# Kernel tuning notes

Measured on AMD Instinct MI355X. Metric: run time of the kernel, lower is better.

Reference implementation:

```python
import jax, jax.numpy as jnp
import numpy as np

B, T, D_IN = 64, 512, 512
D_HID, D_OUT = 1024, 512
NUM_DAYS = 24
EPS = 1e-5


def setup_inputs() -> dict:
    key = jax.random.key(0)
    ks = jax.random.split(key, 8)
    x = jax.random.normal(ks[0], (B, T, D_IN), dtype=jnp.float32)
    day_indices = jax.random.randint(ks[1], (B,), 0, NUM_DAYS)
    s1 = 1.0 / np.sqrt(D_IN)
    s2 = 1.0 / np.sqrt(D_HID)
    W1 = jax.random.uniform(ks[2], (NUM_DAYS, D_IN, D_HID), jnp.float32, -s1, s1)
    b1 = jax.random.uniform(ks[3], (NUM_DAYS, D_HID), jnp.float32, -s1, s1)
    W2 = jax.random.uniform(ks[4], (NUM_DAYS, D_HID, D_OUT), jnp.float32, -s2, s2)
    b2 = jax.random.uniform(ks[5], (NUM_DAYS, D_OUT), jnp.float32, -s2, s2)
    gamma = jnp.ones((NUM_DAYS, D_OUT), jnp.float32)
    beta = jnp.zeros((NUM_DAYS, D_OUT), jnp.float32)
    return {"x": x, "day_indices": day_indices, "W1": W1, "b1": b1,
            "W2": W2, "b2": b2, "gamma": gamma, "beta": beta}


def reference(x, day_indices, W1, b1, W2, b2, gamma, beta):
    # Gather each sample's day-specific adapter params, then one batched pass.
    # Equivalent to the per-day mask/gather/scatter loop in the torch module.
    # Dropout is identity (eval mode).
    W1d = W1[day_indices]                      # [B, D_in, D_hid]
    b1d = b1[day_indices][:, None, :]          # [B, 1, D_hid]
    W2d = W2[day_indices]                      # [B, D_hid, D_out]
    b2d = b2[day_indices][:, None, :]          # [B, 1, D_out]
    h = jax.nn.relu(jnp.einsum('btd,bdh->bth', x, W1d) + b1d)
    y = jnp.einsum('bth,bho->bto', h, W2d) + b2d
    # per-day LayerNorm over last dim
    mean = jnp.mean(y, axis=-1, keepdims=True)
    var = jnp.var(y, axis=-1, keepdims=True)
    y_hat = (y - mean) * jax.lax.rsqrt(var + EPS)
    g = gamma[day_indices][:, None, :]
    bt = beta[day_indices][:, None, :]
    return y_hat * g + bt
```

## Files before the change

kernel.cpp:

```cpp
#include <hip/hip_runtime.h>

#define B_    64
#define T_    512
#define DIN   512
#define DHID  1024
#define DOUT  512
#define NDAYS 24

typedef unsigned short u16;
typedef __bf16 bf16x8 __attribute__((ext_vector_type(8)));
typedef u16    u16x8  __attribute__((ext_vector_type(8)));
typedef float  f32x4  __attribute__((ext_vector_type(4)));

static __device__ __forceinline__ u16 f2bf(float f) {
    union { float f; unsigned u; } v; v.f = f;
    unsigned r = v.u + 0x7FFFu + ((v.u >> 16) & 1u);
    return (u16)(r >> 16);
}
static __device__ __forceinline__ float bf2f(u16 h) {
    union { unsigned u; float f; } v; v.u = ((unsigned)h) << 16;
    return v.f;
}

static __device__ __forceinline__ void gload_lds16(const void* g, void* l) {
    __builtin_amdgcn_global_load_lds(
        (const __attribute__((address_space(1))) void*)g,
        (__attribute__((address_space(3))) void*)l, 16, 0, 0);
}

__global__ __launch_bounds__(256)
void transpose_w(const float* __restrict__ W, u16* __restrict__ WT, int R, int C) {
    __shared__ float t[32][33];
    const int d  = blockIdx.z;
    const int r0 = blockIdx.y * 32, c0 = blockIdx.x * 32;
    const int tx = threadIdx.x, ty = threadIdx.y;
    const float* Wd = W + (size_t)d * R * C;
    u16* WTd = WT + (size_t)d * R * C;
#pragma unroll
    for (int i = 0; i < 4; ++i)
        t[ty + i * 8][tx] = Wd[(size_t)(r0 + ty + i * 8) * C + c0 + tx];
    __syncthreads();
#pragma unroll
    for (int i = 0; i < 4; ++i)
        WTd[(size_t)(c0 + ty + i * 8) * R + r0 + tx] = f2bf(t[tx][ty + i * 8]);
}

__global__ __launch_bounds__(256)
void cvt_bf16(const float* __restrict__ in, u16* __restrict__ outp, int n8) {
    int i = blockIdx.x * 256 + threadIdx.x;
    const int stride = gridDim.x * 256;
    for (; i < n8; i += stride) {
        float4 a = ((const float4*)in)[i * 2];
        float4 b = ((const float4*)in)[i * 2 + 1];
        u16x8 p;
        p[0] = f2bf(a.x); p[1] = f2bf(a.y); p[2] = f2bf(a.z); p[3] = f2bf(a.w);
        p[4] = f2bf(b.x); p[5] = f2bf(b.y); p[6] = f2bf(b.z); p[7] = f2bf(b.w);
        ((u16x8*)outp)[i] = p;
    }
}

template<int MT, int NT, int KT, bool RELU, bool OUT_BF16>
__global__ __launch_bounds__(512, 1)
void gemm8(const u16* __restrict__ Aall,
           const u16* __restrict__ BT,
           const float* __restrict__ bias,
           const int* __restrict__ didx,
           void* __restrict__ Call)
{
    constexpr int GX = MT / 256;
    constexpr int GY = NT / 256;
    constexpr int NWG = GX * GY * B_;
    constexpr int NT_K = KT / 64;
    static_assert(NT_K >= 2 && (NWG % 8) == 0, "geometry");

    constexpr int Q = NWG / 8;
    const int hw = blockIdx.x;
    const int l  = (hw & 7) * Q + (hw >> 3);
    const int bx = l % GX;
    const int by = (l / GX) % GY;
    const int bz = l / (GX * GY);

    const int day = didx[bz];
    const int m0 = bx * 256, n0 = by * 256;
    const int tid = threadIdx.x;
    const int wv = tid >> 6, ln = tid & 63;
    const int wm = wv >> 2, wn = wv & 3;

    __shared__ __align__(16) u16 sA[2][256 * 64];
    __shared__ __align__(16) u16 sB[2][256 * 64];

    const u16* Ab = Aall + (size_t)bz * MT * KT + (size_t)m0 * KT;
    const u16* Bt = BT + (size_t)day * NT * KT + (size_t)n0 * KT;

    auto stageA = [&](int buf, int t, int h) {
#pragma unroll
        for (int c = 0; c < 2; ++c) {
            const int rl = h * 128 + wv * 16 + c * 8 + (ln >> 3);
            const int cd = (ln & 7) ^ (rl & 7);
            gload_lds16(Ab + (size_t)rl * KT + t * 64 + cd * 8,
                        (char*)&sA[buf][(h * 128 + wv * 16 + c * 8) * 64]);
        }
    };
    auto stageB = [&](int buf, int t, int h) {
#pragma unroll
        for (int c = 0; c < 2; ++c) {
            const int rl = h * 128 + wv * 16 + c * 8 + (ln >> 3);
            const int cd = (ln & 7) ^ (rl & 7);
            gload_lds16(Bt + (size_t)rl * KT + t * 64 + cd * 8,
                        (char*)&sB[buf][(h * 128 + wv * 16 + c * 8) * 64]);
        }
    };

    f32x4 acc[8][4];
#pragma unroll
    for (int i = 0; i < 8; ++i)
#pragma unroll
        for (int j = 0; j < 4; ++j)
            acc[i][j] = (f32x4){0.f, 0.f, 0.f, 0.f};

    stageA(0, 0, 0); stageB(0, 0, 0); stageA(0, 0, 1); stageB(0, 0, 1);
    stageA(1, 1, 0); stageB(1, 1, 0);
    asm volatile("s_waitcnt vmcnt(4)" ::: "memory");
    __builtin_amdgcn_s_barrier();

    for (int t = 0; t < NT_K; ++t) {
        const int buf = t & 1;
        const u16* sAb = sA[buf];
        const u16* sBb = sB[buf];
        bf16x8 av[2][4], bv[2][2];

#pragma unroll
        for (int p = 0; p < 4; ++p) {
            const int mq = p >> 1, nq = p & 1;
            if (p == 0 || p == 2) {
#pragma unroll
                for (int ks = 0; ks < 2; ++ks)
#pragma unroll
                    for (int mi = 0; mi < 4; ++mi) {
                        const int r = mq * 128 + wm * 64 + mi * 16 + (ln & 15);
                        const int slot = (ks * 4 + (ln >> 4)) ^ (r & 7);
                        av[ks][mi] = *(const bf16x8*)&sAb[r * 64 + slot * 8];
                    }
            }
#pragma unroll
            for (int ks = 0; ks < 2; ++ks)
#pragma unroll
                for (int ni = 0; ni < 2; ++ni) {
                    const int r = nq * 128 + wn * 32 + ni * 16 + (ln & 15);
                    const int slot = (ks * 4 + (ln >> 4)) ^ (r & 7);
                    bv[ks][ni] = *(const bf16x8*)&sBb[r * 64 + slot * 8];
                }
            if (p == 0)      { if (t + 1 < NT_K) stageA(buf ^ 1, t + 1, 1); }
            else if (p == 1) { if (t + 1 < NT_K) stageB(buf ^ 1, t + 1, 1); }
            else if (p == 2) { if (t + 2 < NT_K) stageA(buf, t + 2, 0); }
            else             { if (t + 2 < NT_K) stageB(buf, t + 2, 0); }

            __builtin_amdgcn_s_barrier();
            asm volatile("s_waitcnt lgkmcnt(0)" ::: "memory");
            __builtin_amdgcn_sched_barrier(0);
            __builtin_amdgcn_s_setprio(1);
#pragma unroll
            for (int ks = 0; ks < 2; ++ks)
#pragma unroll
                for (int mi = 0; mi < 4; ++mi)
#pragma unroll
                    for (int ni = 0; ni < 2; ++ni)
                        acc[mq * 4 + mi][nq * 2 + ni] =
                            __builtin_amdgcn_mfma_f32_16x16x32_bf16(
                                av[ks][mi], bv[ks][ni],
                                acc[mq * 4 + mi][nq * 2 + ni], 0, 0, 0);
            __builtin_amdgcn_s_setprio(0);
            if (p == 3) {
                if (t + 2 < NT_K) asm volatile("s_waitcnt vmcnt(4)" ::: "memory");
                else              asm volatile("s_waitcnt vmcnt(0)" ::: "memory");
            }
            __builtin_amdgcn_s_barrier();
        }
    }

    const float* bs = bias + (size_t)day * NT + n0;
#pragma unroll
    for (int nq = 0; nq < 2; ++nq)
#pragma unroll
        for (int ni = 0; ni < 2; ++ni) {
            const int col = nq * 128 + wn * 32 + ni * 16 + (ln & 15);
            const float bval = bs[col];
#pragma unroll
            for (int mq = 0; mq < 2; ++mq)
#pragma unroll
                for (int mi = 0; mi < 4; ++mi)
#pragma unroll
                    for (int i = 0; i < 4; ++i) {
                        const int row = mq * 128 + wm * 64 + mi * 16 + (ln >> 4) * 4 + i;
                        float v = acc[mq * 4 + mi][nq * 2 + ni][i] + bval;
                        if (RELU) v = fmaxf(v, 0.f);
                        const size_t off = (size_t)bz * MT * NT + (size_t)(m0 + row) * NT + (n0 + col);
                        if (OUT_BF16) ((u16*)Call)[off] = f2bf(v);
                        else          ((float*)Call)[off] = v;
                    }
        }
}

__global__ __launch_bounds__(512, 1)
void gemm2_ln(const u16* __restrict__ Aall,
              const u16* __restrict__ BT,
              const float* __restrict__ bias,
              const int* __restrict__ didx,
              const float* __restrict__ gamma,
              const float* __restrict__ beta,
              float* __restrict__ out)
{
    constexpr int BM = 128, BK = 64;
    constexpr int KT = DHID;
    constexpr int NT_K = KT / BK;
    constexpr int GX = T_ / BM;
    constexpr int NWG = GX * B_;

    constexpr int Q = NWG / 8;
    const int hw = blockIdx.x;
    const int l  = (hw & 7) * Q + (hw >> 3);
    const int bx = l % GX;
    const int bz = l / GX;

    const int day = didx[bz];
    const int m0 = bx * BM;
    const int tid = threadIdx.x;
    const int wv = tid >> 6, ln = tid & 63;
    const int wm = wv >> 2, wn = wv & 3;

    __shared__ __align__(16) u16 sA[2][BM * BK];
    __shared__ __align__(16) u16 sB[2][DOUT * BK];

    const u16* Ab = Aall + (size_t)bz * T_ * KT + (size_t)m0 * KT;
    const u16* Bt = BT + (size_t)day * DOUT * KT;

    auto stageA = [&](int buf, int t) {
#pragma unroll
        for (int c = 0; c < 2; ++c) {
            const int rl = wv * 16 + c * 8 + (ln >> 3);
            const int cd = (ln & 7) ^ (rl & 7);
            gload_lds16(Ab + (size_t)rl * KT + t * BK + cd * 8,
                        (char*)&sA[buf][(wv * 16 + c * 8) * BK]);
        }
    };
    auto stageBh = [&](int buf, int t, int h) {
#pragma unroll
        for (int c = 0; c < 4; ++c) {
            const int rl = h * 256 + wv * 32 + c * 8 + (ln >> 3);
            const int cd = (ln & 7) ^ (rl & 7);
            gload_lds16(Bt + (size_t)rl * KT + t * BK + cd * 8,
                        (char*)&sB[buf][(h * 256 + wv * 32 + c * 8) * BK]);
        }
    };

    f32x4 acc[4][8];
#pragma unroll
    for (int i = 0; i < 4; ++i)
#pragma unroll
        for (int j = 0; j < 8; ++j)
            acc[i][j] = (f32x4){0.f, 0.f, 0.f, 0.f};

    stageA(0, 0); stageBh(0, 0, 0); stageBh(0, 0, 1);
    stageA(1, 1); stageBh(1, 1, 0);
    asm volatile("s_waitcnt vmcnt(6)" ::: "memory");
    __builtin_amdgcn_s_barrier();

    for (int t = 0; t < NT_K; ++t) {
        const int buf = t & 1;
        const u16* sAb = sA[buf];
        const u16* sBb = sB[buf];
        bf16x8 av[2][4], bv[2][2];

#pragma unroll
        for (int p = 0; p < 4; ++p) {
            if (p == 0) {
#pragma unroll
                for (int ks = 0; ks < 2; ++ks)
#pragma unroll
                    for (int mi = 0; mi < 4; ++mi) {
                        const int r = wm * 64 + mi * 16 + (ln & 15);
                        const int slot = (ks * 4 + (ln >> 4)) ^ (r & 7);
                        av[ks][mi] = *(const bf16x8*)&sAb[r * BK + slot * 8];
                    }
            }
#pragma unroll
            for (int ks = 0; ks < 2; ++ks)
#pragma unroll
                for (int ni = 0; ni < 2; ++ni) {
                    const int r = p * 128 + wn * 32 + ni * 16 + (ln & 15);
                    const int slot = (ks * 4 + (ln >> 4)) ^ (r & 7);
                    bv[ks][ni] = *(const bf16x8*)&sBb[r * BK + slot * 8];
                }
            if (p == 0)      { if (t + 1 < NT_K) stageBh(buf ^ 1, t + 1, 1); }
            else if (p == 1) { if (t + 2 < NT_K) stageA(buf, t + 2); }
            else if (p == 2) { if (t + 2 < NT_K) stageBh(buf, t + 2, 0); }

            __builtin_amdgcn_s_barrier();
            asm volatile("s_waitcnt lgkmcnt(0)" ::: "memory");
            __builtin_amdgcn_sched_barrier(0);
            __builtin_amdgcn_s_setprio(1);
#pragma unroll
            for (int ks = 0; ks < 2; ++ks)
#pragma unroll
                for (int mi = 0; mi < 4; ++mi)
#pragma unroll
                    for (int ni = 0; ni < 2; ++ni)
                        acc[mi][p * 2 + ni] =
                            __builtin_amdgcn_mfma_f32_16x16x32_bf16(
                                av[ks][mi], bv[ks][ni], acc[mi][p * 2 + ni], 0, 0, 0);
            __builtin_amdgcn_s_setprio(0);
            if (p == 3) {
                if (t + 2 < NT_K) asm volatile("s_waitcnt vmcnt(6)" ::: "memory");
                else              asm volatile("s_waitcnt vmcnt(0)" ::: "memory");
            }
            __builtin_amdgcn_s_barrier();
        }
    }

    const float* bs = bias + (size_t)day * DOUT;
    float bval[8];
#pragma unroll
    for (int f = 0; f < 8; ++f)
        bval[f] = bs[(f >> 1) * 128 + wn * 32 + (f & 1) * 16 + (ln & 15)];

    u16* yb = (u16*)&sB[0][0];
#pragma unroll
    for (int mi = 0; mi < 4; ++mi)
#pragma unroll
        for (int f = 0; f < 8; ++f) {
            const int col = (f >> 1) * 128 + wn * 32 + (f & 1) * 16 + (ln & 15);
#pragma unroll
            for (int i = 0; i < 4; ++i) {
                const int rloc = wm * 64 + mi * 16 + (ln >> 4) * 4 + i;
                yb[rloc * DOUT + col] = f2bf(acc[mi][f][i] + bval[f]);
            }
        }
    __syncthreads();

    const float* gs = gamma + (size_t)day * DOUT;
    const float* es = beta + (size_t)day * DOUT;
    const float4 g0 = ((const float4*)gs)[ln * 2];
    const float4 g1 = ((const float4*)gs)[ln * 2 + 1];
    const float4 e0 = ((const float4*)es)[ln * 2];
    const float4 e1 = ((const float4*)es)[ln * 2 + 1];

    float* op = out + (size_t)bz * T_ * DOUT + (size_t)m0 * DOUT;
#pragma unroll 4
    for (int r = wv * 16; r < wv * 16 + 16; ++r) {
        const u16x8 yv = *(const u16x8*)&yb[r * DOUT + ln * 8];
        float yf[8];
#pragma unroll
        for (int j = 0; j < 8; ++j) yf[j] = bf2f(yv[j]);
        float s = 0.f, q = 0.f;
#pragma unroll
        for (int j = 0; j < 8; ++j) { s += yf[j]; q += yf[j] * yf[j]; }
#pragma unroll
        for (int o = 32; o; o >>= 1) { s += __shfl_xor(s, o); q += __shfl_xor(q, o); }
        const float mean = s * (1.f / 512.f);
        const float var  = q * (1.f / 512.f) - mean * mean;
        const float rstd = rsqrtf(var + 1e-5f);
        float4 o0, o1;
        o0.x = (yf[0] - mean) * rstd * g0.x + e0.x;
        o0.y = (yf[1] - mean) * rstd * g0.y + e0.y;
        o0.z = (yf[2] - mean) * rstd * g0.z + e0.z;
        o0.w = (yf[3] - mean) * rstd * g0.w + e0.w;
        o1.x = (yf[4] - mean) * rstd * g1.x + e1.x;
        o1.y = (yf[5] - mean) * rstd * g1.y + e1.y;
        o1.z = (yf[6] - mean) * rstd * g1.z + e1.z;
        o1.w = (yf[7] - mean) * rstd * g1.w + e1.w;
        ((float4*)(op + (size_t)r * DOUT))[ln * 2] = o0;
        ((float4*)(op + (size_t)r * DOUT))[ln * 2 + 1] = o1;
    }
}

extern "C" void kernel_launch(void* const* d_in, const int* in_sizes, int n_in,
                              void* d_out, int out_size, void* d_ws, size_t ws_size,
                              hipStream_t stream)
{
    const float* x     = (const float*)d_in[0];
    const int*   didx  = (const int*)d_in[1];
    const float* W1    = (const float*)d_in[2];
    const float* b1    = (const float*)d_in[3];
    const float* W2    = (const float*)d_in[4];
    const float* b2    = (const float*)d_in[5];
    const float* gamma = (const float*)d_in[6];
    const float* beta  = (const float*)d_in[7];
    float* out = (float*)d_out;

    char* ws = (char*)d_ws;
    u16* W1T = (u16*)ws;
    u16* h   = (u16*)(ws + 25165824);
    u16* xb  = (u16*)(ws + 92274688);
    u16* W2T = xb;

    transpose_w<<<dim3(DHID / 32, DIN / 32, NDAYS), dim3(32, 8), 0, stream>>>(W1, W1T, DIN, DHID);
    cvt_bf16<<<2048, 256, 0, stream>>>(x, xb, B_ * T_ * DIN / 8);

    gemm8<T_, DHID, DIN, true, true>
        <<<dim3(2 * 4 * B_), 512, 0, stream>>>(xb, W1T, b1, didx, h);

    transpose_w<<<dim3(DOUT / 32, DHID / 32, NDAYS), dim3(32, 8), 0, stream>>>(W2, W2T, DHID, DOUT);

    gemm2_ln<<<dim3(4 * B_), 512, 0, stream>>>(h, W2T, b2, didx, gamma, beta, out);
}
```

Measured before the change: 155.8 us.

## Fuse fp32-to-bf16 conversion of x into first GEMM's A-tile load path

```diff
diff --git a/kernel.cpp b/kernel.cpp
--- a/kernel.cpp
+++ b/kernel.cpp
@@ -45,33 +45,18 @@
         WTd[(size_t)(c0 + ty + i * 8) * R + r0 + tx] = f2bf(t[tx][ty + i * 8]);
 }
 
-__global__ __launch_bounds__(256)
-void cvt_bf16(const float* __restrict__ in, u16* __restrict__ outp, int n8) {
-    int i = blockIdx.x * 256 + threadIdx.x;
-    const int stride = gridDim.x * 256;
-    for (; i < n8; i += stride) {
-        float4 a = ((const float4*)in)[i * 2];
-        float4 b = ((const float4*)in)[i * 2 + 1];
-        u16x8 p;
-        p[0] = f2bf(a.x); p[1] = f2bf(a.y); p[2] = f2bf(a.z); p[3] = f2bf(a.w);
-        p[4] = f2bf(b.x); p[5] = f2bf(b.y); p[6] = f2bf(b.z); p[7] = f2bf(b.w);
-        ((u16x8*)outp)[i] = p;
-    }
-}
-
-template<int MT, int NT, int KT, bool RELU, bool OUT_BF16>
 __global__ __launch_bounds__(512, 1)
-void gemm8(const u16* __restrict__ Aall,
-           const u16* __restrict__ BT,
-           const float* __restrict__ bias,
-           const int* __restrict__ didx,
-           void* __restrict__ Call)
+void gemm1_x(const float* __restrict__ X,
+             const u16* __restrict__ BT,
+             const float* __restrict__ bias,
+             const int* __restrict__ didx,
+             u16* __restrict__ H)
 {
+    constexpr int MT = T_, NT = DHID, KT = DIN;
     constexpr int GX = MT / 256;
     constexpr int GY = NT / 256;
     constexpr int NWG = GX * GY * B_;
     constexpr int NT_K = KT / 64;
-    static_assert(NT_K >= 2 && (NWG % 8) == 0, "geometry");
 
     constexpr int Q = NWG / 8;
     const int hw = blockIdx.x;
@@ -89,16 +74,35 @@
     __shared__ __align__(16) u16 sA[2][256 * 64];
     __shared__ __align__(16) u16 sB[2][256 * 64];
 
-    const u16* Ab = Aall + (size_t)bz * MT * KT + (size_t)m0 * KT;
+    const float* Af = X + (size_t)bz * MT * KT + (size_t)m0 * KT;
     const u16* Bt = BT + (size_t)day * NT * KT + (size_t)n0 * KT;
 
-    auto stageA = [&](int buf, int t, int h) {
-#pragma unroll
-        for (int c = 0; c < 2; ++c) {
-            const int rl = h * 128 + wv * 16 + c * 8 + (ln >> 3);
-            const int cd = (ln & 7) ^ (rl & 7);
-            gload_lds16(Ab + (size_t)rl * KT + t * 64 + cd * 8,
-                        (char*)&sA[buf][(h * 128 + wv * 16 + c * 8) * 64]);
+    int aR[4], aS[4];
+    const float* aSrc[4];
+#pragma unroll
+    for (int i = 0; i < 4; ++i) {
+        const int chunk = i * 512 + tid;
+        const int r = chunk >> 3, s = chunk & 7, cd = s ^ (r & 7);
+        aR[i] = r; aS[i] = s;
+        aSrc[i] = Af + (size_t)r * KT + cd * 8;
+    }
+    auto loadA = [&](f32x4 a[4][2], int t) {
+#pragma unroll
+        for (int i = 0; i < 4; ++i) {
+            a[i][0] = *(const f32x4*)(aSrc[i] + t * 64);
+            a[i][1] = *(const f32x4*)(aSrc[i] + t * 64 + 4);
+        }
+    };
+    auto writeA = [&](f32x4 a[4][2], int buf) {
+#pragma unroll
+        for (int i = 0; i < 4; ++i) {
+            u16x8 v;
+#pragma unroll
+            for (int j = 0; j < 4; ++j) {
+                v[j]     = f2bf(a[i][0][j]);
+                v[4 + j] = f2bf(a[i][1][j]);
+            }
+            *(u16x8*)&sA[buf][aR[i] * 64 + aS[i] * 8] = v;
         }
     };
     auto stageB = [&](int buf, int t, int h) {
@@ -118,11 +122,18 @@
         for (int j = 0; j < 4; ++j)
             acc[i][j] = (f32x4){0.f, 0.f, 0.f, 0.f};
 
-    stageA(0, 0, 0); stageB(0, 0, 0); stageA(0, 0, 1); stageB(0, 0, 1);
-    stageA(1, 1, 0); stageB(1, 1, 0);
-    asm volatile("s_waitcnt vmcnt(4)" ::: "memory");
+    f32x4 aP[4][2], aQ[4][2];
+    loadA(aP, 0);
+    stageB(0, 0, 0); stageB(0, 0, 1);
+    loadA(aQ, 1);
+    stageB(1, 1, 0);
+    asm volatile("s_waitcnt vmcnt(0)" ::: "memory");
+    writeA(aP, 0);
+    writeA(aQ, 1);
+    asm volatile("s_waitcnt lgkmcnt(0)" ::: "memory");
     __builtin_amdgcn_s_barrier();
 
+    f32x4 aN[4][2];
     for (int t = 0; t < NT_K; ++t) {
         const int buf = t & 1;
         const u16* sAb = sA[buf];
@@ -150,10 +161,9 @@
                     const int slot = (ks * 4 + (ln >> 4)) ^ (r & 7);
                     bv[ks][ni] = *(const bf16x8*)&sBb[r * 64 + slot * 8];
                 }
-            if (p == 0)      { if (t + 1 < NT_K) stageA(buf ^ 1, t + 1, 1); }
-            else if (p == 1) { if (t + 1 < NT_K) stageB(buf ^ 1, t + 1, 1); }
-            else if (p == 2) { if (t + 2 < NT_K) stageA(buf, t + 2, 0); }
-            else             { if (t + 2 < NT_K) stageB(buf, t + 2, 0); }
+            if (p == 0)      { if (t + 1 < NT_K) stageB(buf ^ 1, t + 1, 1); }
+            else if (p == 1) { if (t + 2 < NT_K) loadA(aN, t + 2); }
+            else if (p == 3) { if (t + 2 < NT_K) stageB(buf, t + 2, 0); }
 
             __builtin_amdgcn_s_barrier();
             asm volatile("s_waitcnt lgkmcnt(0)" ::: "memory");
@@ -171,8 +181,12 @@
                                 acc[mq * 4 + mi][nq * 2 + ni], 0, 0, 0);
             __builtin_amdgcn_s_setprio(0);
             if (p == 3) {
-                if (t + 2 < NT_K) asm volatile("s_waitcnt vmcnt(4)" ::: "memory");
-                else              asm volatile("s_waitcnt vmcnt(0)" ::: "memory");
+                if (t + 2 < NT_K) {
+                    asm volatile("s_waitcnt vmcnt(2)" ::: "memory");
+                    writeA(aN, buf);
+                } else {
+                    asm volatile("s_waitcnt vmcnt(0)" ::: "memory");
+                }
             }
             __builtin_amdgcn_s_barrier();
         }
@@ -192,11 +206,8 @@
 #pragma unroll
                     for (int i = 0; i < 4; ++i) {
                         const int row = mq * 128 + wm * 64 + mi * 16 + (ln >> 4) * 4 + i;
-                        float v = acc[mq * 4 + mi][nq * 2 + ni][i] + bval;
-                        if (RELU) v = fmaxf(v, 0.f);
-                        const size_t off = (size_t)bz * MT * NT + (size_t)(m0 + row) * NT + (n0 + col);
-                        if (OUT_BF16) ((u16*)Call)[off] = f2bf(v);
-                        else          ((float*)Call)[off] = v;
+                        const float v = fmaxf(acc[mq * 4 + mi][nq * 2 + ni][i] + bval, 0.f);
+                        H[(size_t)bz * MT * NT + (size_t)(m0 + row) * NT + (n0 + col)] = f2bf(v);
                     }
         }
 }
@@ -390,16 +401,12 @@
     char* ws = (char*)d_ws;
     u16* W1T = (u16*)ws;
     u16* h   = (u16*)(ws + 25165824);
-    u16* xb  = (u16*)(ws + 92274688);
-    u16* W2T = xb;
+    u16* W2T = (u16*)(ws + 92274688);
 
     transpose_w<<<dim3(DHID / 32, DIN / 32, NDAYS), dim3(32, 8), 0, stream>>>(W1, W1T, DIN, DHID);
-    cvt_bf16<<<2048, 256, 0, stream>>>(x, xb, B_ * T_ * DIN / 8);
-
-    gemm8<T_, DHID, DIN, true, true>
-        <<<dim3(2 * 4 * B_), 512, 0, stream>>>(xb, W1T, b1, didx, h);
-
     transpose_w<<<dim3(DOUT / 32, DHID / 32, NDAYS), dim3(32, 8), 0, stream>>>(W2, W2T, DHID, DOUT);
 
+    gemm1_x<<<dim3(2 * 4 * B_), 512, 0, stream>>>(x, W1T, b1, didx, h);
+
     gemm2_ln<<<dim3(4 * B_), 512, 0, stream>>>(h, W2T, b2, didx, gamma, beta, out);
 }
```

Result: slower. 162.9 us (+4.6%).

## Halve GEMM1 K-tile to 32 so two workgroups fit per CU

Applied to the files above, without the earlier changes.

```diff
diff --git a/kernel.cpp b/kernel.cpp
--- a/kernel.cpp
+++ b/kernel.cpp
@@ -60,17 +60,17 @@
 }
 
 template<int MT, int NT, int KT, bool RELU, bool OUT_BF16>
-__global__ __launch_bounds__(512, 1)
-void gemm8(const u16* __restrict__ Aall,
-           const u16* __restrict__ BT,
-           const float* __restrict__ bias,
-           const int* __restrict__ didx,
-           void* __restrict__ Call)
+__global__ __launch_bounds__(512, 2)
+void gemm8k32(const u16* __restrict__ Aall,
+              const u16* __restrict__ BT,
+              const float* __restrict__ bias,
+              const int* __restrict__ didx,
+              void* __restrict__ Call)
 {
     constexpr int GX = MT / 256;
     constexpr int GY = NT / 256;
     constexpr int NWG = GX * GY * B_;
-    constexpr int NT_K = KT / 64;
+    constexpr int NT_K = KT / 32;
     static_assert(NT_K >= 2 && (NWG % 8) == 0, "geometry");
 
     constexpr int Q = NWG / 8;
@@ -86,29 +86,23 @@
     const int wv = tid >> 6, ln = tid & 63;
     const int wm = wv >> 2, wn = wv & 3;
 
-    __shared__ __align__(16) u16 sA[2][256 * 64];
-    __shared__ __align__(16) u16 sB[2][256 * 64];
+    __shared__ __align__(16) u16 sA[2][256 * 32];
+    __shared__ __align__(16) u16 sB[2][256 * 32];
 
     const u16* Ab = Aall + (size_t)bz * MT * KT + (size_t)m0 * KT;
     const u16* Bt = BT + (size_t)day * NT * KT + (size_t)n0 * KT;
 
     auto stageA = [&](int buf, int t, int h) {
-#pragma unroll
-        for (int c = 0; c < 2; ++c) {
-            const int rl = h * 128 + wv * 16 + c * 8 + (ln >> 3);
-            const int cd = (ln & 7) ^ (rl & 7);
-            gload_lds16(Ab + (size_t)rl * KT + t * 64 + cd * 8,
-                        (char*)&sA[buf][(h * 128 + wv * 16 + c * 8) * 64]);
-        }
+        const int rl = h * 128 + wv * 16 + (ln >> 2);
+        const int cd = (ln & 3) ^ (rl & 3);
+        gload_lds16(Ab + (size_t)rl * KT + t * 32 + cd * 8,
+                    (char*)&sA[buf][(h * 128 + wv * 16) * 32]);
     };
     auto stageB = [&](int buf, int t, int h) {
-#pragma unroll
-        for (int c = 0; c < 2; ++c) {
-            const int rl = h * 128 + wv * 16 + c * 8 + (ln >> 3);
-            const int cd = (ln & 7) ^ (rl & 7);
-            gload_lds16(Bt + (size_t)rl * KT + t * 64 + cd * 8,
-                        (char*)&sB[buf][(h * 128 + wv * 16 + c * 8) * 64]);
-        }
+        const int rl = h * 128 + wv * 16 + (ln >> 2);
+        const int cd = (ln & 3) ^ (rl & 3);
+        gload_lds16(Bt + (size_t)rl * KT + t * 32 + cd * 8,
+                    (char*)&sB[buf][(h * 128 + wv * 16) * 32]);
     };
 
     f32x4 acc[8][4];
@@ -120,36 +114,32 @@
 
     stageA(0, 0, 0); stageB(0, 0, 0); stageA(0, 0, 1); stageB(0, 0, 1);
     stageA(1, 1, 0); stageB(1, 1, 0);
-    asm volatile("s_waitcnt vmcnt(4)" ::: "memory");
+    asm volatile("s_waitcnt vmcnt(2)" ::: "memory");
     __builtin_amdgcn_s_barrier();
 
     for (int t = 0; t < NT_K; ++t) {
         const int buf = t & 1;
         const u16* sAb = sA[buf];
         const u16* sBb = sB[buf];
-        bf16x8 av[2][4], bv[2][2];
+        bf16x8 av[4], bv[2];
 
 #pragma unroll
         for (int p = 0; p < 4; ++p) {
             const int mq = p >> 1, nq = p & 1;
             if (p == 0 || p == 2) {
 #pragma unroll
-                for (int ks = 0; ks < 2; ++ks)
-#pragma unroll
-                    for (int mi = 0; mi < 4; ++mi) {
-                        const int r = mq * 128 + wm * 64 + mi * 16 + (ln & 15);
-                        const int slot = (ks * 4 + (ln >> 4)) ^ (r & 7);
-                        av[ks][mi] = *(const bf16x8*)&sAb[r * 64 + slot * 8];
-                    }
-            }
-#pragma unroll
-            for (int ks = 0; ks < 2; ++ks)
-#pragma unroll
-                for (int ni = 0; ni < 2; ++ni) {
-                    const int r = nq * 128 + wn * 32 + ni * 16 + (ln & 15);
-                    const int slot = (ks * 4 + (ln >> 4)) ^ (r & 7);
-                    bv[ks][ni] = *(const bf16x8*)&sBb[r * 64 + slot * 8];
+                for (int mi = 0; mi < 4; ++mi) {
+                    const int r = mq * 128 + wm * 64 + mi * 16 + (ln & 15);
+                    const int slot = (ln >> 4) ^ (r & 3);
+                    av[mi] = *(const bf16x8*)&sAb[r * 32 + slot * 8];
                 }
+            }
+#pragma unroll
+            for (int ni = 0; ni < 2; ++ni) {
+                const int r = nq * 128 + wn * 32 + ni * 16 + (ln & 15);
+                const int slot = (ln >> 4) ^ (r & 3);
+                bv[ni] = *(const bf16x8*)&sBb[r * 32 + slot * 8];
+            }
             if (p == 0)      { if (t + 1 < NT_K) stageA(buf ^ 1, t + 1, 1); }
             else if (p == 1) { if (t + 1 < NT_K) stageB(buf ^ 1, t + 1, 1); }
             else if (p == 2) { if (t + 2 < NT_K) stageA(buf, t + 2, 0); }
@@ -160,18 +150,16 @@
             __builtin_amdgcn_sched_barrier(0);
             __builtin_amdgcn_s_setprio(1);
 #pragma unroll
-            for (int ks = 0; ks < 2; ++ks)
-#pragma unroll
-                for (int mi = 0; mi < 4; ++mi)
-#pragma unroll
-                    for (int ni = 0; ni < 2; ++ni)
-                        acc[mq * 4 + mi][nq * 2 + ni] =
-                            __builtin_amdgcn_mfma_f32_16x16x32_bf16(
-                                av[ks][mi], bv[ks][ni],
-                                acc[mq * 4 + mi][nq * 2 + ni], 0, 0, 0);
+            for (int mi = 0; mi < 4; ++mi)
+#pragma unroll
+                for (int ni = 0; ni < 2; ++ni)
+                    acc[mq * 4 + mi][nq * 2 + ni] =
+                        __builtin_amdgcn_mfma_f32_16x16x32_bf16(
+                            av[mi], bv[ni],
+                            acc[mq * 4 + mi][nq * 2 + ni], 0, 0, 0);
             __builtin_amdgcn_s_setprio(0);
             if (p == 3) {
-                if (t + 2 < NT_K) asm volatile("s_waitcnt vmcnt(4)" ::: "memory");
+                if (t + 2 < NT_K) asm volatile("s_waitcnt vmcnt(2)" ::: "memory");
                 else              asm volatile("s_waitcnt vmcnt(0)" ::: "memory");
             }
             __builtin_amdgcn_s_barrier();
@@ -396,7 +384,7 @@
     transpose_w<<<dim3(DHID / 32, DIN / 32, NDAYS), dim3(32, 8), 0, stream>>>(W1, W1T, DIN, DHID);
     cvt_bf16<<<2048, 256, 0, stream>>>(x, xb, B_ * T_ * DIN / 8);
 
-    gemm8<T_, DHID, DIN, true, true>
+    gemm8k32<T_, DHID, DIN, true, true>
         <<<dim3(2 * 4 * B_), 512, 0, stream>>>(xb, W1T, b1, didx, h);
 
     transpose_w<<<dim3(DOUT / 32, DHID / 32, NDAYS), dim3(32, 8), 0, stream>>>(W2, W2T, DHID, DOUT);
```

Result: no change. 156.2 us (+0.2%).

## Shrink gemm2_ln tiles to 64x512 with 256 threads and two blocks per CU

Applied to the files above, without the earlier changes.

```diff
diff --git a/kernel.cpp b/kernel.cpp
--- a/kernel.cpp
+++ b/kernel.cpp
@@ -201,7 +201,7 @@
         }
 }
 
-__global__ __launch_bounds__(512, 1)
+__global__ __launch_bounds__(256, 2)
 void gemm2_ln(const u16* __restrict__ Aall,
               const u16* __restrict__ BT,
               const float* __restrict__ bias,
@@ -210,7 +210,7 @@
               const float* __restrict__ beta,
               float* __restrict__ out)
 {
-    constexpr int BM = 128, BK = 64;
+    constexpr int BM = 64, BK = 32;
     constexpr int KT = DHID;
     constexpr int NT_K = KT / BK;
     constexpr int GX = T_ / BM;
@@ -226,7 +226,7 @@
     const int m0 = bx * BM;
     const int tid = threadIdx.x;
     const int wv = tid >> 6, ln = tid & 63;
-    const int wm = wv >> 2, wn = wv & 3;
+    const int wn = wv;
 
     __shared__ __align__(16) u16 sA[2][BM * BK];
     __shared__ __align__(16) u16 sB[2][DOUT * BK];
@@ -235,21 +235,18 @@
     const u16* Bt = BT + (size_t)day * DOUT * KT;
 
     auto stageA = [&](int buf, int t) {
-#pragma unroll
-        for (int c = 0; c < 2; ++c) {
-            const int rl = wv * 16 + c * 8 + (ln >> 3);
-            const int cd = (ln & 7) ^ (rl & 7);
-            gload_lds16(Ab + (size_t)rl * KT + t * BK + cd * 8,
-                        (char*)&sA[buf][(wv * 16 + c * 8) * BK]);
-        }
+        const int rl = wv * 16 + (ln >> 2);
+        const int cd = (ln & 3) ^ ((rl >> 1) & 3);
+        gload_lds16(Ab + (size_t)rl * KT + t * BK + cd * 8,
+                    (char*)&sA[buf][(wv * 16) * BK]);
     };
     auto stageBh = [&](int buf, int t, int h) {
 #pragma unroll
         for (int c = 0; c < 4; ++c) {
-            const int rl = h * 256 + wv * 32 + c * 8 + (ln >> 3);
-            const int cd = (ln & 7) ^ (rl & 7);
+            const int rl = h * 256 + c * 64 + wv * 16 + (ln >> 2);
+            const int cd = (ln & 3) ^ ((rl >> 1) & 3);
             gload_lds16(Bt + (size_t)rl * KT + t * BK + cd * 8,
-                        (char*)&sB[buf][(h * 256 + wv * 32 + c * 8) * BK]);
+                        (char*)&sB[buf][(h * 256 + c * 64 + wv * 16) * BK]);
         }
     };
 
@@ -262,35 +259,31 @@
 
     stageA(0, 0); stageBh(0, 0, 0); stageBh(0, 0, 1);
     stageA(1, 1); stageBh(1, 1, 0);
-    asm volatile("s_waitcnt vmcnt(6)" ::: "memory");
+    asm volatile("s_waitcnt vmcnt(5)" ::: "memory");
     __builtin_amdgcn_s_barrier();
 
     for (int t = 0; t < NT_K; ++t) {
         const int buf = t & 1;
         const u16* sAb = sA[buf];
         const u16* sBb = sB[buf];
-        bf16x8 av[2][4], bv[2][2];
+        bf16x8 av[4], bv[2];
 
 #pragma unroll
         for (int p = 0; p < 4; ++p) {
             if (p == 0) {
 #pragma unroll
-                for (int ks = 0; ks < 2; ++ks)
-#pragma unroll
-                    for (int mi = 0; mi < 4; ++mi) {
-                        const int r = wm * 64 + mi * 16 + (ln & 15);
-                        const int slot = (ks * 4 + (ln >> 4)) ^ (r & 7);
-                        av[ks][mi] = *(const bf16x8*)&sAb[r * BK + slot * 8];
-                    }
-            }
-#pragma unroll
-            for (int ks = 0; ks < 2; ++ks)
-#pragma unroll
-                for (int ni = 0; ni < 2; ++ni) {
-                    const int r = p * 128 + wn * 32 + ni * 16 + (ln & 15);
-                    const int slot = (ks * 4 + (ln >> 4)) ^ (r & 7);
-                    bv[ks][ni] = *(const bf16x8*)&sBb[r * BK + slot * 8];
+                for (int mi = 0; mi < 4; ++mi) {
+                    const int r = mi * 16 + (ln & 15);
+                    const int slot = (ln >> 4) ^ ((r >> 1) & 3);
+                    av[mi] = *(const bf16x8*)&sAb[r * BK + slot * 8];
                 }
+            }
+#pragma unroll
+            for (int ni = 0; ni < 2; ++ni) {
+                const int r = p * 128 + wn * 32 + ni * 16 + (ln & 15);
+                const int slot = (ln >> 4) ^ ((r >> 1) & 3);
+                bv[ni] = *(const bf16x8*)&sBb[r * BK + slot * 8];
+            }
             if (p == 0)      { if (t + 1 < NT_K) stageBh(buf ^ 1, t + 1, 1); }
             else if (p == 1) { if (t + 2 < NT_K) stageA(buf, t + 2); }
             else if (p == 2) { if (t + 2 < NT_K) stageBh(buf, t + 2, 0); }
@@ -300,17 +293,15 @@
             __builtin_amdgcn_sched_barrier(0);
             __builtin_amdgcn_s_setprio(1);
 #pragma unroll
-            for (int ks = 0; ks < 2; ++ks)
-#pragma unroll
-                for (int mi = 0; mi < 4; ++mi)
-#pragma unroll
-                    for (int ni = 0; ni < 2; ++ni)
-                        acc[mi][p * 2 + ni] =
-                            __builtin_amdgcn_mfma_f32_16x16x32_bf16(
-                                av[ks][mi], bv[ks][ni], acc[mi][p * 2 + ni], 0, 0, 0);
+            for (int mi = 0; mi < 4; ++mi)
+#pragma unroll
+                for (int ni = 0; ni < 2; ++ni)
+                    acc[mi][p * 2 + ni] =
+                        __builtin_amdgcn_mfma_f32_16x16x32_bf16(
+                            av[mi], bv[ni], acc[mi][p * 2 + ni], 0, 0, 0);
             __builtin_amdgcn_s_setprio(0);
             if (p == 3) {
-                if (t + 2 < NT_K) asm volatile("s_waitcnt vmcnt(6)" ::: "memory");
+                if (t + 2 < NT_K) asm volatile("s_waitcnt vmcnt(5)" ::: "memory");
                 else              asm volatile("s_waitcnt vmcnt(0)" ::: "memory");
             }
             __builtin_amdgcn_s_barrier();
@@ -331,7 +322,7 @@
             const int col = (f >> 1) * 128 + wn * 32 + (f & 1) * 16 + (ln & 15);
 #pragma unroll
             for (int i = 0; i < 4; ++i) {
-                const int rloc = wm * 64 + mi * 16 + (ln >> 4) * 4 + i;
+                const int rloc = mi * 16 + (ln >> 4) * 4 + i;
                 yb[rloc * DOUT + col] = f2bf(acc[mi][f][i] + bval[f]);
             }
         }
@@ -401,5 +392,5 @@
 
     transpose_w<<<dim3(DOUT / 32, DHID / 32, NDAYS), dim3(32, 8), 0, stream>>>(W2, W2T, DHID, DOUT);
 
-    gemm2_ln<<<dim3(4 * B_), 512, 0, stream>>>(h, W2T, b2, didx, gamma, beta, out);
-}
+    gemm2_ln<<<dim3(8 * B_), 256, 0, stream>>>(h, W2T, b2, didx, gamma, beta, out);
+}
```

Result: slower. 163.0 us (+4.6%).
